# Kernel optimization log

Hardware: AMD Instinct MI355X
Metric: run time of the kernel (lower is better)

The kernel has to match this reference:

```python
import jax, jax.numpy as jnp
import numpy as np

B, N, D = 2, 2048, 768
H = 12
DH = D // H
SCALE = DH ** -0.5


def setup_inputs() -> dict:
    key = jax.random.key(0)
    k1, k2, k3 = jax.random.split(key, 3)
    x = jax.random.normal(k1, (B, N, D), dtype=jnp.float32)
    w_qkv = jax.random.normal(k2, (D, 3 * D), dtype=jnp.float32) * (D ** -0.5)
    b_qkv = jnp.zeros((3 * D,), dtype=jnp.float32)
    w_proj = jax.random.normal(k3, (D, D), dtype=jnp.float32) * (D ** -0.5)
    b_proj = jnp.zeros((D,), dtype=jnp.float32)
    return {"x": x, "w_qkv": w_qkv, "b_qkv": b_qkv, "w_proj": w_proj, "b_proj": b_proj}


def reference(x, w_qkv, b_qkv, w_proj, b_proj):
    b, n, d = x.shape
    # qkv: (B, n, 3, H, DH) -> (3, B, H, n, DH)
    qkv = (x @ w_qkv + b_qkv).reshape(b, n, 3, H, DH).transpose(2, 0, 3, 1, 4)
    q, k, v = qkv[0], qkv[1], qkv[2]
    # naive full attention matrix (B, H, n, n)
    attn = jnp.einsum('bhqd,bhkd->bhqk', q, k) * SCALE
    attn = jax.nn.softmax(attn, axis=-1)
    out = jnp.einsum('bhqk,bhkd->bhqd', attn, v)  # (B, H, n, DH)
    out = out.transpose(0, 2, 1, 3).reshape(b, n, d)
    return out @ w_proj + b_proj
```

## Files before the change

### kernel.cpp

```cpp
#include <hip/hip_runtime.h>


#define CB 2
#define CN 2048
#define CD 768
#define CH 12
#define CDH 64
#define CEXPSCALE 0.18033688f

typedef __bf16 bf16x8 __attribute__((ext_vector_type(8)));
typedef float f32x4 __attribute__((ext_vector_type(4)));
typedef unsigned short u16x8 __attribute__((ext_vector_type(8)));

static __device__ __forceinline__ unsigned short f2bf(float f) {
  union { float f; unsigned u; } v; v.f = f;
  unsigned r = v.u + 0x7fffu + ((v.u >> 16) & 1u);
  return (unsigned short)(r >> 16);
}

static __device__ __forceinline__ void gld_lds16(const unsigned short* g, unsigned short* lds_base) {
  __builtin_amdgcn_global_load_lds(
      (const __attribute__((address_space(1))) unsigned int*)g,
      (__attribute__((address_space(3))) unsigned int*)(unsigned int)(unsigned long long)lds_base,
      16, 0, 0);
}

__global__ __launch_bounds__(256) void prep(const float* __restrict__ x,
                                            unsigned short* __restrict__ xb,
                                            const float* __restrict__ w_qkv,
                                            unsigned short* __restrict__ wqkv_t,
                                            const float* __restrict__ w_proj,
                                            unsigned short* __restrict__ wproj_t) {
  __shared__ __align__(16) unsigned short t[64][72];
  const int bid = blockIdx.x, tid = threadIdx.x;
#pragma unroll
  for (int it = 0; it < 2; ++it) {
    size_t i = ((size_t)(bid * 2 + it) * 256 + tid) * 8;
    f32x4 a = *(const f32x4*)&x[i];
    f32x4 b = *(const f32x4*)&x[i + 4];
    u16x8 o;
#pragma unroll
    for (int j = 0; j < 4; ++j) { o[j] = f2bf(a[j]); o[4 + j] = f2bf(b[j]); }
    *(u16x8*)&xb[i] = o;
  }
  if (bid >= 576) return;
  const float* src; unsigned short* dst; int R, C, c0, r0;
  if (bid < 432) { src = w_qkv; dst = wqkv_t; R = 768; C = 2304; c0 = (bid % 36) * 64; r0 = (bid / 36) * 64; }
  else { int u = bid - 432; src = w_proj; dst = wproj_t; R = 768; C = 768; c0 = (u % 12) * 64; r0 = (u / 12) * 64; }
#pragma unroll
  for (int i = 0; i < 4; ++i) {
    int c = tid + i * 256;
    int row = c >> 4, cc = (c & 15) * 4;
    f32x4 v = *(const f32x4*)&src[(size_t)(r0 + row) * C + c0 + cc];
#pragma unroll
    for (int j = 0; j < 4; ++j) t[row][cc + j] = f2bf(v[j]);
  }
  __syncthreads();
#pragma unroll
  for (int i = 0; i < 2; ++i) {
    int c = tid + i * 256;
    int drow = c >> 3, rc = (c & 7) * 8;
    u16x8 v;
#pragma unroll
    for (int j = 0; j < 8; ++j) v[j] = t[rc + j][drow];
    *(u16x8*)&dst[(size_t)(c0 + drow) * R + r0 + rc] = v;
  }
}

extern __shared__ __align__(16) unsigned short smem[];

template <int TM, int TN>
__global__ __launch_bounds__(256, 4) void gemm_db(const unsigned short* __restrict__ A,
                                                  const unsigned short* __restrict__ Bt,
                                                  const float* __restrict__ bias,
                                                  int M, int N, int K, int mode,
                                                  unsigned short* __restrict__ o0,
                                                  unsigned short* __restrict__ o1,
                                                  unsigned short* __restrict__ o2,
                                                  float* __restrict__ outF) {
  constexpr int NT = TN / 32;
  unsigned short* As = smem;
  unsigned short* Bs = smem + 2 * TM * 32;
  unsigned short* Ct = smem;
  const int tid = threadIdx.x;
  const int w = tid >> 6, lane = tid & 63, quad = lane >> 4, lc = lane & 15;
  const int wm = (w >> 1) * 32, wn = (w & 1) * (TN / 2);
  const int row0 = blockIdx.y * TM, col0 = blockIdx.x * TN;
  f32x4 acc[2][NT] = {};

  const int rl = lane >> 2, cl = lane & 3;
  const int gc = cl ^ ((rl >> 1) & 3);
  const int rsw = (lc >> 1) & 3;
  const int nk = K / 32;

  auto stage = [&](int kt, int buf) {
    const int k0 = kt * 32;
    gld_lds16(&A[(size_t)(row0 + w * 16 + rl) * K + k0 + gc * 8],
              &As[buf * (TM * 32) + (w * 16) * 32]);
#pragma unroll
    for (int jb = 0; jb < TN / 64; ++jb)
      gld_lds16(&Bt[(size_t)(col0 + w * (TN / 4) + jb * 16 + rl) * K + k0 + gc * 8],
                &Bs[buf * (TN * 32) + (w * (TN / 4) + jb * 16) * 32]);
  };

  stage(0, 0);
  for (int kt = 0; kt < nk; ++kt) {
    const int bb = kt & 1;
    __syncthreads();
    if (kt + 1 < nk) stage(kt + 1, bb ^ 1);
    bf16x8 af[2], bfv[NT];
#pragma unroll
    for (int mt = 0; mt < 2; ++mt)
      af[mt] = *(const bf16x8*)&As[bb * (TM * 32) + (wm + mt * 16 + lc) * 32 + (quad ^ rsw) * 8];
#pragma unroll
    for (int nt = 0; nt < NT; ++nt)
      bfv[nt] = *(const bf16x8*)&Bs[bb * (TN * 32) + (wn + nt * 16 + lc) * 32 + (quad ^ rsw) * 8];
#pragma unroll
    for (int mt = 0; mt < 2; ++mt)
#pragma unroll
      for (int nt = 0; nt < NT; ++nt)
        acc[mt][nt] = __builtin_amdgcn_mfma_f32_16x16x32_bf16(af[mt], bfv[nt], acc[mt][nt], 0, 0, 0);
  }

  if (mode == 0 && col0 >= 1536) {
    __syncthreads();
#pragma unroll
    for (int mt = 0; mt < 2; ++mt) {
#pragma unroll
      for (int nt = 0; nt < NT; ++nt) {
        int jl = wn + nt * 16 + lc;
        int il0 = wm + mt * 16 + quad * 4;
        float bj = bias[col0 + jl];
        unsigned short a0 = f2bf(acc[mt][nt][0] + bj);
        unsigned short a1 = f2bf(acc[mt][nt][1] + bj);
        unsigned short a2 = f2bf(acc[mt][nt][2] + bj);
        unsigned short a3 = f2bf(acc[mt][nt][3] + bj);
        uint2 dd;
        dd.x = (unsigned)a0 | ((unsigned)a1 << 16);
        dd.y = (unsigned)a2 | ((unsigned)a3 << 16);
        *(uint2*)&Ct[jl * (TM + 8) + il0] = dd;
      }
    }
    __syncthreads();
    const int b = row0 >> 11, n0 = row0 & 2047;
    constexpr int CPR = TM / 8;
#pragma unroll
    for (int i = 0; i < (TN * CPR) / 256; ++i) {
      int c = tid + i * 256;
      int jl = c / CPR, cc = (c % CPR) * 8;
      u16x8 v = *(const u16x8*)&Ct[jl * (TM + 8) + cc];
      int jcol = col0 - 1536 + jl;
      int h = jcol >> 6, d = jcol & 63;
      size_t gr = ((size_t)(b * CH + h) * CDH + d);
      *(u16x8*)&o2[gr * CN + n0 + cc] = v;
    }
  } else {
#pragma unroll
    for (int mt = 0; mt < 2; ++mt) {
#pragma unroll
      for (int nt = 0; nt < NT; ++nt) {
#pragma unroll
        for (int r = 0; r < 4; ++r) {
          int i = row0 + wm + mt * 16 + quad * 4 + r;
          int j = col0 + wn + nt * 16 + lc;
          float v = acc[mt][nt][r] + bias[j];
          if (mode == 0) {
            int b = i >> 11, n = i & 2047;
            int sec = (j >= 768) ? 1 : 0;
            int within = j - sec * 768;
            int h = within >> 6, d = within & 63;
            int bh = b * CH + h;
            if (sec == 0) o0[((size_t)bh * CN + n) * CDH + d] = f2bf(v * CEXPSCALE);
            else          o1[((size_t)bh * CN + n) * CDH + d] = f2bf(v);
          } else {
            outF[(size_t)i * N + j] = v;
          }
        }
      }
    }
  }
}

__global__ __launch_bounds__(256, 4) void attn64(const unsigned short* __restrict__ Q,
                                                 const unsigned short* __restrict__ K,
                                                 const unsigned short* __restrict__ Vt,
                                                 unsigned short* __restrict__ O) {
  __shared__ __align__(16) unsigned short Kls[2][64 * 64];
  __shared__ __align__(16) unsigned short Vls[2][64 * 64];
  const int bh = blockIdx.x, qt0 = blockIdx.y;
  const int tid = threadIdx.x;
  const int w = tid >> 6, lane = tid & 63, quad = lane >> 4, lc = lane & 15;
  const unsigned short* Qb = Q + (size_t)bh * CN * CDH;
  const unsigned short* Kb = K + (size_t)bh * CN * CDH;
  const unsigned short* Vb = Vt + (size_t)bh * CDH * CN;
  const int q0w = qt0 * 64 + w * 16;

  const int sr = lane >> 3, sc = lane & 7;
  const int sg = sc ^ sr;
  const int ksw = lc & 7;
  const int c0 = (quad ^ ksw) * 8;
  const int c1 = ((4 | quad) ^ ksw) * 8;

  int ks[2];
#pragma unroll
  for (int j2 = 0; j2 < 2; ++j2) {
    int s = (w * 2 + j2) * 8 + sr;
    ks[j2] = ((s & 28) << 1) | ((s & 32) >> 3) | (s & 3);
  }

  bf16x8 qf[2];
#pragma unroll
  for (int hh = 0; hh < 2; ++hh)
    qf[hh] = *(const bf16x8*)&Qb[(size_t)(q0w + lc) * CDH + hh * 32 + quad * 8];

  f32x4 o[4] = {};
  float rs = 0.f;

#pragma unroll
  for (int j2 = 0; j2 < 2; ++j2) {
    int j = w * 2 + j2;
    int r = j * 8 + sr;
    gld_lds16(&Kb[(size_t)ks[j2] * CDH + sg * 8], &Kls[0][j * 8 * 64]);
    gld_lds16(&Vb[(size_t)r * CN + 0 + sg * 8], &Vls[0][j * 8 * 64]);
  }

  for (int kt = 0; kt < CN / 64; ++kt) {
    const int bb = kt & 1;
    __syncthreads();
    if (kt + 1 < CN / 64) {
      const int kn = (kt + 1) * 64;
#pragma unroll
      for (int j2 = 0; j2 < 2; ++j2) {
        int j = w * 2 + j2;
        int r = j * 8 + sr;
        gld_lds16(&Kb[(size_t)(kn + ks[j2]) * CDH + sg * 8], &Kls[bb ^ 1][j * 8 * 64]);
        gld_lds16(&Vb[(size_t)r * CN + kn + sg * 8], &Vls[bb ^ 1][j * 8 * 64]);
      }
    }
    bf16x8 kf[4][2];
#pragma unroll
    for (int kvt = 0; kvt < 4; ++kvt) {
      const int row = (kvt * 16 + lc) * 64;
      kf[kvt][0] = *(const bf16x8*)&Kls[bb][row + c0];
      kf[kvt][1] = *(const bf16x8*)&Kls[bb][row + c1];
    }
    bf16x8 vf[4][2];
#pragma unroll
    for (int dt = 0; dt < 4; ++dt) {
      const int row = (dt * 16 + lc) * 64;
      vf[dt][0] = *(const bf16x8*)&Vls[bb][row + c0];
      vf[dt][1] = *(const bf16x8*)&Vls[bb][row + c1];
    }
    f32x4 z[4] = {};
    __builtin_amdgcn_s_setprio(1);
#pragma unroll
    for (int kvt = 0; kvt < 4; ++kvt) {
      z[kvt] = __builtin_amdgcn_mfma_f32_16x16x32_bf16(kf[kvt][0], qf[0], z[kvt], 0, 0, 0);
      z[kvt] = __builtin_amdgcn_mfma_f32_16x16x32_bf16(kf[kvt][1], qf[1], z[kvt], 0, 0, 0);
    }
    __builtin_amdgcn_s_setprio(0);
    union PU { unsigned u[4]; bf16x8 v; } P0, P1;
#pragma unroll
    for (int g = 0; g < 2; ++g) {
      unsigned pu[4];
#pragma unroll
      for (int hpair = 0; hpair < 2; ++hpair) {
        const int kvt = hpair * 2 + g;
        float e0 = exp2f(z[kvt][0]);
        float e1 = exp2f(z[kvt][1]);
        float e2 = exp2f(z[kvt][2]);
        float e3 = exp2f(z[kvt][3]);
        rs += (e0 + e1) + (e2 + e3);
        pu[hpair * 2]     = __builtin_amdgcn_perm(__float_as_uint(e1), __float_as_uint(e0), 0x07060302u);
        pu[hpair * 2 + 1] = __builtin_amdgcn_perm(__float_as_uint(e3), __float_as_uint(e2), 0x07060302u);
      }
      if (g == 0) { P0.u[0] = pu[0]; P0.u[1] = pu[1]; P0.u[2] = pu[2]; P0.u[3] = pu[3]; }
      else        { P1.u[0] = pu[0]; P1.u[1] = pu[1]; P1.u[2] = pu[2]; P1.u[3] = pu[3]; }
    }
    __builtin_amdgcn_s_setprio(1);
#pragma unroll
    for (int dt = 0; dt < 4; ++dt) {
      o[dt] = __builtin_amdgcn_mfma_f32_16x16x32_bf16(P0.v, vf[dt][0], o[dt], 0, 0, 0);
      o[dt] = __builtin_amdgcn_mfma_f32_16x16x32_bf16(P1.v, vf[dt][1], o[dt], 0, 0, 0);
    }
    __builtin_amdgcn_s_setprio(0);
  }

  rs += __shfl_xor(rs, 16, 64);
  rs += __shfl_xor(rs, 32, 64);
  const int b = bh / CH, h = bh - b * CH;
#pragma unroll
  for (int r = 0; r < 4; ++r) {
    float lr = __shfl(rs, quad * 4 + r, 64);
    float inv = 1.0f / lr;
    int i = b * CN + q0w + quad * 4 + r;
#pragma unroll
    for (int dt = 0; dt < 4; ++dt) {
      int j = h * CDH + dt * 16 + lc;
      O[(size_t)i * CD + j] = f2bf(o[dt][r] * inv);
    }
  }
}

extern "C" void kernel_launch(void* const* d_in, const int* in_sizes, int n_in,
                              void* d_out, int out_size, void* d_ws, size_t ws_size,
                              hipStream_t stream) {
  const float* x      = (const float*)d_in[0];
  const float* w_qkv  = (const float*)d_in[1];
  const float* b_qkv  = (const float*)d_in[2];
  const float* w_proj = (const float*)d_in[3];
  const float* b_proj = (const float*)d_in[4];
  float* out = (float*)d_out;
  unsigned short* ws = (unsigned short*)d_ws;

  unsigned short* xb      = ws;
  unsigned short* wqkv_t  = xb + (size_t)4096 * 768;
  unsigned short* wproj_t = wqkv_t + (size_t)2304 * 768;
  unsigned short* Qs  = wproj_t + (size_t)768 * 768;
  unsigned short* Ks  = Qs  + (size_t)CB * CH * CN * CDH;
  unsigned short* Vts = Ks  + (size_t)CB * CH * CN * CDH;
  unsigned short* AO  = Vts + (size_t)CB * CH * CN * CDH;

  const size_t smem_qkv  = (size_t)2 * (64 + 128) * 32 * 2;
  const size_t smem_proj = (size_t)2 * (64 + 64) * 32 * 2;

  prep<<<768, 256, 0, stream>>>(x, xb, w_qkv, wqkv_t, w_proj, wproj_t);
  gemm_db<64, 128><<<dim3(2304 / 128, 4096 / 64), 256, smem_qkv, stream>>>(
      xb, wqkv_t, b_qkv, 4096, 2304, 768, 0, Qs, Ks, Vts, nullptr);
  attn64<<<dim3(CB * CH, CN / 64), 256, 0, stream>>>(Qs, Ks, Vts, AO);
  gemm_db<64, 64><<<dim3(768 / 64, 4096 / 64), 256, smem_proj, stream>>>(
      AO, wproj_t, b_proj, 4096, 768, 768, 1, nullptr, nullptr, nullptr, out);
}
```

Measured before the change: 168.2 us.

## Software-pipeline PV MFMA one tile behind QK and use raw exp2 intrinsic

Restructures the attention inner loop so the P·V MFMAs for the previous KV tile are issued at the start of the next iteration. This lets them overlap with the K loads and the QK MFMAs, and a final epilogue drains the last tile. V fragments and P are kept in registers across iterations, initialised to zero for the first pass. Also replaces exp2f with the hardware exp2 builtin and relaxes launch bounds from 4 to 3 waves to make room for the extra registers. The cost is lower occupancy.

```diff
diff --git a/kernel.cpp b/kernel.cpp
--- a/kernel.cpp
+++ b/kernel.cpp
@@ -181,7 +181,7 @@
   }
 }
 
-__global__ __launch_bounds__(256, 4) void attn64(const unsigned short* __restrict__ Q,
+__global__ __launch_bounds__(256, 3) void attn64(const unsigned short* __restrict__ Q,
                                                  const unsigned short* __restrict__ K,
                                                  const unsigned short* __restrict__ Vt,
                                                  unsigned short* __restrict__ O) {
@@ -216,6 +216,13 @@
   f32x4 o[4] = {};
   float rs = 0.f;
 
+  union PU { unsigned u[4]; bf16x8 v; } P0p, P1p;
+  P0p.u[0] = P0p.u[1] = P0p.u[2] = P0p.u[3] = 0;
+  P1p = P0p;
+  bf16x8 vfp[4][2];
+#pragma unroll
+  for (int dt = 0; dt < 4; ++dt) { vfp[dt][0] = P0p.v; vfp[dt][1] = P0p.v; }
+
 #pragma unroll
   for (int j2 = 0; j2 < 2; ++j2) {
     int j = w * 2 + j2;
@@ -237,6 +244,13 @@
         gld_lds16(&Vb[(size_t)r * CN + kn + sg * 8], &Vls[bb ^ 1][j * 8 * 64]);
       }
     }
+    __builtin_amdgcn_s_setprio(1);
+#pragma unroll
+    for (int dt = 0; dt < 4; ++dt) {
+      o[dt] = __builtin_amdgcn_mfma_f32_16x16x32_bf16(P0p.v, vfp[dt][0], o[dt], 0, 0, 0);
+      o[dt] = __builtin_amdgcn_mfma_f32_16x16x32_bf16(P1p.v, vfp[dt][1], o[dt], 0, 0, 0);
+    }
+    __builtin_amdgcn_s_setprio(0);
     bf16x8 kf[4][2];
 #pragma unroll
     for (int kvt = 0; kvt < 4; ++kvt) {
@@ -244,13 +258,6 @@
       kf[kvt][0] = *(const bf16x8*)&Kls[bb][row + c0];
       kf[kvt][1] = *(const bf16x8*)&Kls[bb][row + c1];
     }
-    bf16x8 vf[4][2];
-#pragma unroll
-    for (int dt = 0; dt < 4; ++dt) {
-      const int row = (dt * 16 + lc) * 64;
-      vf[dt][0] = *(const bf16x8*)&Vls[bb][row + c0];
-      vf[dt][1] = *(const bf16x8*)&Vls[bb][row + c1];
-    }
     f32x4 z[4] = {};
     __builtin_amdgcn_s_setprio(1);
 #pragma unroll
@@ -259,32 +266,38 @@
       z[kvt] = __builtin_amdgcn_mfma_f32_16x16x32_bf16(kf[kvt][1], qf[1], z[kvt], 0, 0, 0);
     }
     __builtin_amdgcn_s_setprio(0);
-    union PU { unsigned u[4]; bf16x8 v; } P0, P1;
+#pragma unroll
+    for (int dt = 0; dt < 4; ++dt) {
+      const int row = (dt * 16 + lc) * 64;
+      vfp[dt][0] = *(const bf16x8*)&Vls[bb][row + c0];
+      vfp[dt][1] = *(const bf16x8*)&Vls[bb][row + c1];
+    }
 #pragma unroll
     for (int g = 0; g < 2; ++g) {
       unsigned pu[4];
 #pragma unroll
       for (int hpair = 0; hpair < 2; ++hpair) {
         const int kvt = hpair * 2 + g;
-        float e0 = exp2f(z[kvt][0]);
-        float e1 = exp2f(z[kvt][1]);
-        float e2 = exp2f(z[kvt][2]);
-        float e3 = exp2f(z[kvt][3]);
+        float e0 = __builtin_amdgcn_exp2f(z[kvt][0]);
+        float e1 = __builtin_amdgcn_exp2f(z[kvt][1]);
+        float e2 = __builtin_amdgcn_exp2f(z[kvt][2]);
+        float e3 = __builtin_amdgcn_exp2f(z[kvt][3]);
         rs += (e0 + e1) + (e2 + e3);
         pu[hpair * 2]     = __builtin_amdgcn_perm(__float_as_uint(e1), __float_as_uint(e0), 0x07060302u);
         pu[hpair * 2 + 1] = __builtin_amdgcn_perm(__float_as_uint(e3), __float_as_uint(e2), 0x07060302u);
       }
-      if (g == 0) { P0.u[0] = pu[0]; P0.u[1] = pu[1]; P0.u[2] = pu[2]; P0.u[3] = pu[3]; }
-      else        { P1.u[0] = pu[0]; P1.u[1] = pu[1]; P1.u[2] = pu[2]; P1.u[3] = pu[3]; }
-    }
-    __builtin_amdgcn_s_setprio(1);
-#pragma unroll
-    for (int dt = 0; dt < 4; ++dt) {
-      o[dt] = __builtin_amdgcn_mfma_f32_16x16x32_bf16(P0.v, vf[dt][0], o[dt], 0, 0, 0);
-      o[dt] = __builtin_amdgcn_mfma_f32_16x16x32_bf16(P1.v, vf[dt][1], o[dt], 0, 0, 0);
-    }
-    __builtin_amdgcn_s_setprio(0);
-  }
+      if (g == 0) { P0p.u[0] = pu[0]; P0p.u[1] = pu[1]; P0p.u[2] = pu[2]; P0p.u[3] = pu[3]; }
+      else        { P1p.u[0] = pu[0]; P1p.u[1] = pu[1]; P1p.u[2] = pu[2]; P1p.u[3] = pu[3]; }
+    }
+  }
+
+  __builtin_amdgcn_s_setprio(1);
+#pragma unroll
+  for (int dt = 0; dt < 4; ++dt) {
+    o[dt] = __builtin_amdgcn_mfma_f32_16x16x32_bf16(P0p.v, vfp[dt][0], o[dt], 0, 0, 0);
+    o[dt] = __builtin_amdgcn_mfma_f32_16x16x32_bf16(P1p.v, vfp[dt][1], o[dt], 0, 0, 0);
+  }
+  __builtin_amdgcn_s_setprio(0);
 
   rs += __shfl_xor(rs, 16, 64);
   rs += __shfl_xor(rs, 32, 64);
```

Measured after the change: 159.8 us (median of 2 runs). 1.05x faster.
